# Performance work log

Hardware: AMD Instinct MI355X
Metric: run time of the kernel (lower is better)

Reference implementation:

```python
import jax, jax.numpy as jnp
import numpy as np

N_NODES = 100000
N_EDGES = 800000
D_IN = 128
D_H = 512


def _glorot(key, shape):
    fan_in, fan_out = shape[1], shape[0]
    lim = jnp.sqrt(6.0 / (fan_in + fan_out))
    return jax.random.uniform(key, shape, jnp.float32, -lim, lim)


def setup_inputs() -> dict:
    key = jax.random.key(0)
    ks = jax.random.split(key, 16)
    x = jax.random.normal(ks[0], (N_NODES, D_IN), jnp.float32)
    edge_index = jax.random.randint(ks[1], (2, N_EDGES), 0, N_NODES, jnp.int64)
    return {
        "x": x,
        "edge_index": edge_index,
        # SAGEConv layer1: lin_l (neighbors, with bias), lin_r (root, no bias)
        "Wl1": _glorot(ks[2], (D_H, D_IN)), "bl1": jnp.zeros((D_H,), jnp.float32),
        "Wr1": _glorot(ks[3], (D_H, D_IN)),
        # SAGEConv layer2
        "Wl2": _glorot(ks[4], (D_H, D_H)), "bl2": jnp.zeros((D_H,), jnp.float32),
        "Wr2": _glorot(ks[5], (D_H, D_H)),
        # SAGEConv layer3
        "Wl3": _glorot(ks[6], (D_H, D_H)), "bl3": jnp.zeros((D_H,), jnp.float32),
        "Wr3": _glorot(ks[7], (D_H, D_H)),
        # residual projections W, W2 (nn.Linear with bias)
        "Ww": _glorot(ks[8], (D_H, D_IN)), "bw": jnp.zeros((D_H,), jnp.float32),
        "Ww2": _glorot(ks[9], (D_H, D_IN)), "bw2": jnp.zeros((D_H,), jnp.float32),
        # shared PReLU parameter (nn.PReLU default: single param init 0.25)
        "a": jnp.array(0.25, jnp.float32),
    }


def _prelu(x, a):
    return jnp.where(x > 0, x, a * x)


def _sage_conv(x, src, dst, Wl, bl, Wr):
    # mean-aggregate neighbor features x[src] onto dst, then linear + root term
    msg = jax.ops.segment_sum(x[src], dst, num_segments=N_NODES)  # [N, d]
    deg = jax.ops.segment_sum(jnp.ones((src.shape[0],), x.dtype), dst,
                              num_segments=N_NODES)
    agg = msg / jnp.maximum(deg, 1.0)[:, None]
    return agg @ Wl.T + bl + x @ Wr.T


def reference(x, edge_index, Wl1, bl1, Wr1, Wl2, bl2, Wr2, Wl3, bl3, Wr3,
              Ww, bw, Ww2, bw2, a):
    src, dst = edge_index[0], edge_index[1]
    h1 = _prelu(_sage_conv(x, src, dst, Wl1, bl1, Wr1), a)
    h2 = _prelu(_sage_conv(h1 + (x @ Ww.T + bw), src, dst, Wl2, bl2, Wr2), a)
    h3 = _prelu(_sage_conv(h2 + h1 + (x @ Ww2.T + bw2), src, dst, Wl3, bl3, Wr3), a)
    return h3
```

## Files before the change

### kernel.cpp

```cpp
#include <hip/hip_runtime.h>
#include <stddef.h>

#define NN 100000
#define NE 800000
#define DIN 128
#define DH 512
#define MT 782
#define NWG (MT * 4)
#define CPX (NWG / 8)

typedef __attribute__((ext_vector_type(8))) short sh8;
typedef __attribute__((ext_vector_type(4))) float f32x4;

__device__ __forceinline__ unsigned short f2b(float f) {
  unsigned u = __float_as_uint(f);
  return (unsigned short)((u + 0x7FFFu + ((u >> 16) & 1u)) >> 16);
}
__device__ __forceinline__ float b2f(unsigned short s) {
  return __uint_as_float(((unsigned)s) << 16);
}

__device__ __forceinline__ void gload16(const unsigned short* g, unsigned short* l) {
  __builtin_amdgcn_global_load_lds(
      (const __attribute__((address_space(1))) void*)g,
      (__attribute__((address_space(3))) void*)l, 16, 0, 0);
}

#define SCHED_FENCE() __builtin_amdgcn_sched_barrier(0)
#define VMCNT(n) asm volatile("s_waitcnt vmcnt(" #n ")" ::: "memory")


__global__ void k_count(const int* __restrict__ dst, int* __restrict__ cnt) {
  int i = blockIdx.x * blockDim.x + threadIdx.x;
  if (i < NE) atomicAdd(&cnt[dst[i]], 1);
}

__global__ void k_invdeg(const int* __restrict__ cnt, float* __restrict__ inv_deg) {
  int i = blockIdx.x * blockDim.x + threadIdx.x;
  if (i < NN) inv_deg[i] = 1.0f / (float)(cnt[i] > 1 ? cnt[i] : 1);
}

__global__ void k_scan1(const int* __restrict__ cnt, int* __restrict__ excl,
                        int* __restrict__ partials) {
  __shared__ int sh[256];
  int tid = threadIdx.x;
  int base = blockIdx.x * 1024 + tid * 4;
  int v[4]; int s = 0;
#pragma unroll
  for (int i = 0; i < 4; i++) { int idx = base + i; v[i] = (idx < NN) ? cnt[idx] : 0; s += v[i]; }
  sh[tid] = s; __syncthreads();
  for (int off = 1; off < 256; off <<= 1) {
    int t = (tid >= off) ? sh[tid - off] : 0;
    __syncthreads();
    sh[tid] += t;
    __syncthreads();
  }
  int run = sh[tid] - s;
#pragma unroll
  for (int i = 0; i < 4; i++) { int idx = base + i; if (idx < NN) excl[idx] = run; run += v[i]; }
  if (tid == 255) partials[blockIdx.x] = sh[255];
}

__global__ void k_scan2(int* __restrict__ partials, int* __restrict__ row_start, int nparts) {
  __shared__ int sh[128];
  int tid = threadIdx.x;
  int v = (tid < nparts) ? partials[tid] : 0;
  sh[tid] = v; __syncthreads();
  for (int off = 1; off < 128; off <<= 1) {
    int t = (tid >= off) ? sh[tid - off] : 0;
    __syncthreads();
    sh[tid] += t;
    __syncthreads();
  }
  if (tid < nparts) partials[tid] = sh[tid] - v;
  if (tid == 127) row_start[NN] = sh[127];
}

__global__ void k_scan3(int* __restrict__ excl, const int* __restrict__ partials) {
  int i = blockIdx.x * blockDim.x + threadIdx.x;
  if (i < NN) excl[i] += partials[i >> 10];
}

__global__ void k_fill(const int* __restrict__ src, const int* __restrict__ dst,
                       const int* __restrict__ row_start, int* __restrict__ cursor,
                       int* __restrict__ ssrc) {
  int i = blockIdx.x * blockDim.x + threadIdx.x;
  if (i < NE) {
    int d = dst[i];
    int pos = atomicAdd(&cursor[d], 1);
    ssrc[row_start[d] + pos] = src[i];
  }
}


__global__ void k_f2b(const float* __restrict__ src, unsigned short* __restrict__ dst, int n) {
  int i = (blockIdx.x * blockDim.x + threadIdx.x) * 4;
  if (i < n) {
    float4 v = *(const float4*)(src + i);
    ushort4 o;
    o.x = f2b(v.x); o.y = f2b(v.y); o.z = f2b(v.z); o.w = f2b(v.w);
    *(ushort4*)(dst + i) = o;
  }
}


__global__ __launch_bounds__(256) void k_aggb512(
    const unsigned short* __restrict__ z, const int* __restrict__ rs,
    const int* __restrict__ ssrc, const float* __restrict__ inv_deg,
    unsigned short* __restrict__ agg) {
  int w = (blockIdx.x * blockDim.x + threadIdx.x) >> 6;
  int lane = threadIdx.x & 63;
  if (w >= NN) return;
  int e0 = rs[w], e1 = rs[w + 1];
  float acc[8] = {0, 0, 0, 0, 0, 0, 0, 0};
  int e = e0;
  for (; e + 1 < e1; e += 2) {
    int sa = ssrc[e], sb = ssrc[e + 1];
    sh8 va = *(const sh8*)(z + (size_t)sa * DH + lane * 8);
    sh8 vb = *(const sh8*)(z + (size_t)sb * DH + lane * 8);
#pragma unroll
    for (int j = 0; j < 8; ++j) acc[j] += b2f((unsigned short)va[j]) + b2f((unsigned short)vb[j]);
  }
  if (e < e1) {
    int sa = ssrc[e];
    sh8 va = *(const sh8*)(z + (size_t)sa * DH + lane * 8);
#pragma unroll
    for (int j = 0; j < 8; ++j) acc[j] += b2f((unsigned short)va[j]);
  }
  float s0 = inv_deg[w];
  sh8 o;
#pragma unroll
  for (int j = 0; j < 8; ++j) o[j] = (short)f2b(acc[j] * s0);
  *(sh8*)(agg + (size_t)w * DH + lane * 8) = o;
}

__global__ __launch_bounds__(256) void k_aggb128(
    const unsigned short* __restrict__ z, const int* __restrict__ rs,
    const int* __restrict__ ssrc, const float* __restrict__ inv_deg,
    unsigned short* __restrict__ agg) {
  int w = (blockIdx.x * blockDim.x + threadIdx.x) >> 6;
  int lane = threadIdx.x & 63;
  if (w >= NN) return;
  int e0 = rs[w], e1 = rs[w + 1];
  float a0 = 0.f, a1 = 0.f;
  int e = e0;
  for (; e + 1 < e1; e += 2) {
    int sa = ssrc[e], sb = ssrc[e + 1];
    unsigned va = *(const unsigned*)(z + (size_t)sa * DIN + lane * 2);
    unsigned vb = *(const unsigned*)(z + (size_t)sb * DIN + lane * 2);
    a0 += b2f((unsigned short)(va & 0xFFFFu)) + b2f((unsigned short)(vb & 0xFFFFu));
    a1 += b2f((unsigned short)(va >> 16)) + b2f((unsigned short)(vb >> 16));
  }
  if (e < e1) {
    unsigned va = *(const unsigned*)(z + (size_t)ssrc[e] * DIN + lane * 2);
    a0 += b2f((unsigned short)(va & 0xFFFFu));
    a1 += b2f((unsigned short)(va >> 16));
  }
  float s0 = inv_deg[w];
  unsigned o = (unsigned)f2b(a0 * s0) | ((unsigned)f2b(a1 * s0) << 16);
  *(unsigned*)(agg + (size_t)w * DIN + lane * 2) = o;
}


__device__ __forceinline__ void stage_tile(
    unsigned short* ldsA, unsigned short* ldsB,
    const unsigned short* __restrict__ A, int sA, int m0,
    const unsigned short* __restrict__ B, int sB, int n0,
    int k0, int tid) {
  const int w = tid >> 6, l = tid & 63;
  const int kc = (l & 3) * 8;
  const int rsub = l >> 2;
#pragma unroll
  for (int i = 0; i < 2; ++i) {
    int rl = w * 32 + i * 16 + rsub;
    int ra = m0 + rl; if (ra >= NN) ra = NN - 1;
    gload16(A + (size_t)ra * sA + k0 + kc, ldsA + (size_t)(w * 32 + i * 16) * 32);
    gload16(B + (size_t)(n0 + rl) * sB + k0 + kc, ldsB + (size_t)(w * 32 + i * 16) * 32);
  }
}

__device__ __forceinline__ void mfma_step(
    const unsigned short* As, const unsigned short* Bs,
    int wr, int wc, int r16, int kg, f32x4 (&acc)[4][4]) {
  sh8 af[4], bf[4];
#pragma unroll
  for (int i = 0; i < 4; ++i)
    af[i] = *(const sh8*)&As[(wr + i * 16 + r16) * 32 + kg * 8];
#pragma unroll
  for (int j = 0; j < 4; ++j)
    bf[j] = *(const sh8*)&Bs[(wc + j * 16 + r16) * 32 + kg * 8];
#pragma unroll
  for (int i = 0; i < 4; ++i)
#pragma unroll
    for (int j = 0; j < 4; ++j)
      acc[i][j] = __builtin_amdgcn_mfma_f32_16x16x32_bf16(af[i], bf[j], acc[i][j], 0, 0, 0);
}

#define PIPE_WAIT(s, S)                 \
  do {                                  \
    if ((s) < (S) - 2) VMCNT(8);        \
    else if ((s) == (S) - 2) VMCNT(4);  \
    else VMCNT(0);                      \
    SCHED_FENCE();                      \
    __builtin_amdgcn_s_barrier();       \
    SCHED_FENCE();                      \
  } while (0)

#define PIPE_END()                      \
  do {                                  \
    SCHED_FENCE();                      \
    __builtin_amdgcn_s_barrier();       \
    SCHED_FENCE();                      \
  } while (0)

__global__ __launch_bounds__(256, 2) void k_gemm1(
    const unsigned short* __restrict__ ag, const unsigned short* __restrict__ xb,
    const unsigned short* __restrict__ Wl1, const unsigned short* __restrict__ Wr1,
    const unsigned short* __restrict__ Ww, const unsigned short* __restrict__ Ww2,
    const float* __restrict__ bl1, const float* __restrict__ bw,
    const float* __restrict__ bw2, const float* __restrict__ aptr,
    unsigned short* __restrict__ z2o, unsigned short* __restrict__ z3po) {
  __shared__ __align__(16) unsigned short As[3][128 * 32];
  __shared__ __align__(16) unsigned short Bs[3][128 * 32];
  const int tid = threadIdx.x;
  const int b = blockIdx.x;
  const int L = (b & 7) * CPX + (b >> 3);
  const int m0 = (L >> 2) * 128, n0 = (L & 3) * 128;
  const int wid = tid >> 6, lane = tid & 63;
  const int r16 = lane & 15, kg = lane >> 4;
  const int wr = (wid >> 1) * 64, wc = (wid & 1) * 64;

  f32x4 a0[4][4], a1[4][4], a2[4][4];
#pragma unroll
  for (int i = 0; i < 4; ++i)
#pragma unroll
    for (int j = 0; j < 4; ++j) { a0[i][j] = 0.f; a1[i][j] = 0.f; a2[i][j] = 0.f; }

  auto stage = [&](int s, int buf) {
    const int seg = s >> 2, k0 = (s & 3) * 32;
    const unsigned short* Ap = (seg == 0) ? ag : xb;
    const unsigned short* Bp = (seg == 0) ? Wl1 : (seg == 1) ? Wr1 : (seg == 2) ? Ww : Ww2;
    stage_tile(As[buf], Bs[buf], Ap, DIN, m0, Bp, DIN, n0, k0, tid);
  };

  stage(0, 0);
  stage(1, 1);
  int cur = 0, nxt = 2;
  for (int s = 0; s < 16; ++s) {
    if (s + 2 < 16) stage(s + 2, nxt);
    PIPE_WAIT(s, 16);
    const int seg = s >> 2;
    __builtin_amdgcn_s_setprio(1);
    if (seg <= 1)      mfma_step(As[cur], Bs[cur], wr, wc, r16, kg, a0);
    else if (seg == 2) mfma_step(As[cur], Bs[cur], wr, wc, r16, kg, a1);
    else               mfma_step(As[cur], Bs[cur], wr, wc, r16, kg, a2);
    __builtin_amdgcn_s_setprio(0);
    PIPE_END();
    cur = (cur == 2) ? 0 : cur + 1;
    nxt = (nxt == 2) ? 0 : nxt + 1;
  }

  const float aval = aptr[0];
#pragma unroll
  for (int i = 0; i < 4; ++i) {
    const int mbase = m0 + wr + i * 16 + kg * 4;
#pragma unroll
    for (int j = 0; j < 4; ++j) {
      const int col = n0 + wc + j * 16 + r16;
      const float b1 = bl1[col], b2 = bw[col], b3 = bw2[col];
#pragma unroll
      for (int r = 0; r < 4; ++r) {
        const int m = mbase + r;
        if (m >= NN) continue;
        float h1 = a0[i][j][r] + b1;
        h1 = h1 > 0.f ? h1 : aval * h1;
        z2o[(size_t)m * DH + col] = f2b(h1 + a1[i][j][r] + b2);
        z3po[(size_t)m * DH + col] = f2b(h1 + a2[i][j][r] + b3);
      }
    }
  }
}

template <bool LAST>
__global__ __launch_bounds__(256, 3) void k_gemm23(
    const unsigned short* __restrict__ Aag, const unsigned short* __restrict__ Az,
    const unsigned short* __restrict__ Wl, const unsigned short* __restrict__ Wr,
    const float* __restrict__ bl, const float* __restrict__ aptr,
    const unsigned short* __restrict__ z3p, void* __restrict__ outp) {
  __shared__ __align__(16) unsigned short As[3][128 * 32];
  __shared__ __align__(16) unsigned short Bs[3][128 * 32];
  const int tid = threadIdx.x;
  const int b = blockIdx.x;
  const int L = (b & 7) * CPX + (b >> 3);
  const int m0 = (L >> 2) * 128, n0 = (L & 3) * 128;
  const int wid = tid >> 6, lane = tid & 63;
  const int r16 = lane & 15, kg = lane >> 4;
  const int wr = (wid >> 1) * 64, wc = (wid & 1) * 64;

  f32x4 acc[4][4];
#pragma unroll
  for (int i = 0; i < 4; ++i)
#pragma unroll
    for (int j = 0; j < 4; ++j) acc[i][j] = 0.f;

  auto stage = [&](int s, int buf) {
    const int k0 = (s & 15) * 32;
    const unsigned short* Ap = (s < 16) ? Aag : Az;
    const unsigned short* Bp = (s < 16) ? Wl : Wr;
    stage_tile(As[buf], Bs[buf], Ap, DH, m0, Bp, DH, n0, k0, tid);
  };

  stage(0, 0);
  stage(1, 1);
  int cur = 0, nxt = 2;
  for (int s = 0; s < 32; ++s) {
    if (s + 2 < 32) stage(s + 2, nxt);
    PIPE_WAIT(s, 32);
    __builtin_amdgcn_s_setprio(1);
    mfma_step(As[cur], Bs[cur], wr, wc, r16, kg, acc);
    __builtin_amdgcn_s_setprio(0);
    PIPE_END();
    cur = (cur == 2) ? 0 : cur + 1;
    nxt = (nxt == 2) ? 0 : nxt + 1;
  }

  const float aval = aptr[0];
  float* outf = (float*)outp;
  unsigned short* outb = (unsigned short*)outp;
#pragma unroll
  for (int i = 0; i < 4; ++i) {
    const int mbase = m0 + wr + i * 16 + kg * 4;
#pragma unroll
    for (int j = 0; j < 4; ++j) {
      const int col = n0 + wc + j * 16 + r16;
      const float bv = bl[col];
#pragma unroll
      for (int r = 0; r < 4; ++r) {
        const int m = mbase + r;
        if (m >= NN) continue;
        float h = acc[i][j][r] + bv;
        h = h > 0.f ? h : aval * h;
        if constexpr (LAST) {
          outf[(size_t)m * DH + col] = h;
        } else {
          outb[(size_t)m * DH + col] = f2b(h + b2f(z3p[(size_t)m * DH + col]));
        }
      }
    }
  }
}


extern "C" void kernel_launch(void* const* d_in, const int* in_sizes, int n_in,
                              void* d_out, int out_size, void* d_ws, size_t ws_size,
                              hipStream_t stream) {
  const float* x = (const float*)d_in[0];
  const int* ei = (const int*)d_in[1];
  const float* Wl1 = (const float*)d_in[2];
  const float* bl1 = (const float*)d_in[3];
  const float* Wr1 = (const float*)d_in[4];
  const float* Wl2 = (const float*)d_in[5];
  const float* bl2 = (const float*)d_in[6];
  const float* Wr2 = (const float*)d_in[7];
  const float* Wl3 = (const float*)d_in[8];
  const float* bl3 = (const float*)d_in[9];
  const float* Wr3 = (const float*)d_in[10];
  const float* Ww  = (const float*)d_in[11];
  const float* bw  = (const float*)d_in[12];
  const float* Ww2 = (const float*)d_in[13];
  const float* bw2 = (const float*)d_in[14];
  const float* ap  = (const float*)d_in[15];
  float* out = (float*)d_out;

  const size_t MP = 100096;
  char* w = (char*)d_ws;
  size_t off = 0;
  unsigned short* xb   = (unsigned short*)(w + off); off += MP * DIN * 2;
  unsigned short* ag1  = (unsigned short*)(w + off); off += MP * DIN * 2;
  unsigned short* agb  = (unsigned short*)(w + off); off += MP * DH * 2;
  unsigned short* zb   = (unsigned short*)(w + off); off += MP * DH * 2;
  unsigned short* zc   = (unsigned short*)(w + off); off += MP * DH * 2;
  unsigned short* z3pb = (unsigned short*)(w + off); off += MP * DH * 2;
  unsigned short* Wl1b = (unsigned short*)(w + off); off += (size_t)DH * DIN * 2;
  unsigned short* Wr1b = (unsigned short*)(w + off); off += (size_t)DH * DIN * 2;
  unsigned short* Wwb  = (unsigned short*)(w + off); off += (size_t)DH * DIN * 2;
  unsigned short* Ww2b = (unsigned short*)(w + off); off += (size_t)DH * DIN * 2;
  unsigned short* Wl2b = (unsigned short*)(w + off); off += (size_t)DH * DH * 2;
  unsigned short* Wr2b = (unsigned short*)(w + off); off += (size_t)DH * DH * 2;
  unsigned short* Wl3b = (unsigned short*)(w + off); off += (size_t)DH * DH * 2;
  unsigned short* Wr3b = (unsigned short*)(w + off); off += (size_t)DH * DH * 2;
  float* inv_deg = (float*)(w + off); off += (size_t)NN * 4;
  int* row_start = (int*)(w + off); off += (size_t)(NN + 1) * 4;
  int* cursor = (int*)(w + off); off += (size_t)NN * 4;
  int* ssrc = (int*)(w + off); off += (size_t)NE * 4;
  int* partials = (int*)(w + off); off += 512;

  const int* esrc = ei;
  const int* edst = ei + NE;

  hipMemsetAsync(cursor, 0, NN * 4, stream);
  k_count<<<(NE + 255) / 256, 256, 0, stream>>>(edst, cursor);
  k_invdeg<<<(NN + 255) / 256, 256, 0, stream>>>(cursor, inv_deg);
  k_scan1<<<(NN + 1023) / 1024, 256, 0, stream>>>(cursor, row_start, partials);
  k_scan2<<<1, 128, 0, stream>>>(partials, row_start, (NN + 1023) / 1024);
  k_scan3<<<(NN + 255) / 256, 256, 0, stream>>>(row_start, partials);
  hipMemsetAsync(cursor, 0, NN * 4, stream);
  k_fill<<<(NE + 255) / 256, 256, 0, stream>>>(esrc, edst, row_start, cursor, ssrc);

  const int WK = DH * DIN;
  const int WB = DH * DH;
  k_f2b<<<(WK / 4 + 255) / 256, 256, 0, stream>>>(Wl1, Wl1b, WK);
  k_f2b<<<(WK / 4 + 255) / 256, 256, 0, stream>>>(Wr1, Wr1b, WK);
  k_f2b<<<(WK / 4 + 255) / 256, 256, 0, stream>>>(Ww,  Wwb,  WK);
  k_f2b<<<(WK / 4 + 255) / 256, 256, 0, stream>>>(Ww2, Ww2b, WK);
  k_f2b<<<(WB / 4 + 255) / 256, 256, 0, stream>>>(Wl2, Wl2b, WB);
  k_f2b<<<(WB / 4 + 255) / 256, 256, 0, stream>>>(Wr2, Wr2b, WB);
  k_f2b<<<(WB / 4 + 255) / 256, 256, 0, stream>>>(Wl3, Wl3b, WB);
  k_f2b<<<(WB / 4 + 255) / 256, 256, 0, stream>>>(Wr3, Wr3b, WB);
  k_f2b<<<(NN * DIN / 4 + 255) / 256, 256, 0, stream>>>(x, xb, NN * DIN);

  k_aggb128<<<(NN + 3) / 4, 256, 0, stream>>>(xb, row_start, ssrc, inv_deg, ag1);
  k_gemm1<<<NWG, 256, 0, stream>>>(ag1, xb, Wl1b, Wr1b, Wwb, Ww2b, bl1, bw, bw2, ap,
                                   zb, z3pb);
  k_aggb512<<<(NN + 3) / 4, 256, 0, stream>>>(zb, row_start, ssrc, inv_deg, agb);
  k_gemm23<false><<<NWG, 256, 0, stream>>>(agb, zb, Wl2b, Wr2b, bl2, ap, z3pb, zc);
  k_aggb512<<<(NN + 3) / 4, 256, 0, stream>>>(zc, row_start, ssrc, inv_deg, agb);
  k_gemm23<true><<<NWG, 256, 0, stream>>>(agb, zc, Wl3b, Wr3b, bl3, ap, nullptr, out);
}
```

Measured before the change: 1.005 ms.

## Rewrite layer-2/3 GEMM as 256x256-tile 8-wave kernel with swizzled LDS

Replaces the 128x128, 4-wave, triple-buffered GEMM for layers 2 and 3 with a 256x256-tile, 8-wave (512-thread) kernel that uses double-buffered LDS with an XOR-swizzled layout. Each wave computes 128x64 in two halves, and the next stage's global-to-LDS loads are issued between the two MFMA halves. The goal is to raise arithmetic intensity per loaded byte, cut LDS bank conflicts, and remap workgroups evenly across the 8 XCDs. The trade-offs are more accumulator registers (8x4 f32x4 per wave), lower occupancy, and a larger padded workspace.

```diff
diff --git a/kernel.cpp b/kernel.cpp
--- a/kernel.cpp
+++ b/kernel.cpp
@@ -6,8 +6,8 @@
 #define DIN 128
 #define DH 512
 #define MT 782
-#define NWG (MT * 4)
-#define CPX (NWG / 8)
+#define NWG1 (MT * 4)
+#define CPX1 (NWG1 / 8)
 
 typedef __attribute__((ext_vector_type(8))) short sh8;
 typedef __attribute__((ext_vector_type(4))) float f32x4;
@@ -27,7 +27,9 @@
 }
 
 #define SCHED_FENCE() __builtin_amdgcn_sched_barrier(0)
+#define MEM_FENCE() asm volatile("" ::: "memory")
 #define VMCNT(n) asm volatile("s_waitcnt vmcnt(" #n ")" ::: "memory")
+#define LGKM0() asm volatile("s_waitcnt lgkmcnt(0)" ::: "memory")
 
 
 __global__ void k_count(const int* __restrict__ dst, int* __restrict__ cnt) {
@@ -203,14 +205,14 @@
     else VMCNT(0);                      \
     SCHED_FENCE();                      \
     __builtin_amdgcn_s_barrier();       \
-    SCHED_FENCE();                      \
+    MEM_FENCE(); SCHED_FENCE();         \
   } while (0)
 
 #define PIPE_END()                      \
   do {                                  \
     SCHED_FENCE();                      \
     __builtin_amdgcn_s_barrier();       \
-    SCHED_FENCE();                      \
+    MEM_FENCE(); SCHED_FENCE();         \
   } while (0)
 
 __global__ __launch_bounds__(256, 2) void k_gemm1(
@@ -224,7 +226,7 @@
   __shared__ __align__(16) unsigned short Bs[3][128 * 32];
   const int tid = threadIdx.x;
   const int b = blockIdx.x;
-  const int L = (b & 7) * CPX + (b >> 3);
+  const int L = (b & 7) * CPX1 + (b >> 3);
   const int m0 = (L >> 2) * 128, n0 = (L & 3) * 128;
   const int wid = tid >> 6, lane = tid & 63;
   const int r16 = lane & 15, kg = lane >> 4;
@@ -281,58 +283,110 @@
   }
 }
 
+
+#define TILE_E 8192
+#define NT23 32
+
+__device__ __forceinline__ void stage_u(const unsigned short* __restrict__ src,
+                                        int ld, int row0, int rowmax, int k0,
+                                        unsigned short* lds, int u, int l) {
+  int p = u * 8 + (l >> 3);
+  int v = (l & 7) ^ (p & 7);
+  int r = row0 + 2 * p + (v >> 2);
+  if (r > rowmax) r = rowmax;
+  gload16(src + (size_t)r * ld + k0 + (v & 3) * 8, lds + u * 512);
+}
+
+__device__ __forceinline__ sh8 frag(const unsigned short* lds, int r, int kg) {
+  int p = r >> 1;
+  int s = (((r & 1) << 2) | kg) ^ (p & 7);
+  return *(const sh8*)(lds + p * 64 + s * 8);
+}
+
 template <bool LAST>
-__global__ __launch_bounds__(256, 3) void k_gemm23(
+__global__ __launch_bounds__(512) void k8_gemm23(
     const unsigned short* __restrict__ Aag, const unsigned short* __restrict__ Az,
     const unsigned short* __restrict__ Wl, const unsigned short* __restrict__ Wr,
     const float* __restrict__ bl, const float* __restrict__ aptr,
     const unsigned short* __restrict__ z3p, void* __restrict__ outp) {
-  __shared__ __align__(16) unsigned short As[3][128 * 32];
-  __shared__ __align__(16) unsigned short Bs[3][128 * 32];
-  const int tid = threadIdx.x;
+  __shared__ __align__(16) unsigned short LA[2][TILE_E];
+  __shared__ __align__(16) unsigned short LB[2][TILE_E];
   const int b = blockIdx.x;
-  const int L = (b & 7) * CPX + (b >> 3);
-  const int m0 = (L >> 2) * 128, n0 = (L & 3) * 128;
-  const int wid = tid >> 6, lane = tid & 63;
-  const int r16 = lane & 15, kg = lane >> 4;
-  const int wr = (wid >> 1) * 64, wc = (wid & 1) * 64;
-
-  f32x4 acc[4][4];
-#pragma unroll
-  for (int i = 0; i < 4; ++i)
+  const int xcd = b & 7, lo = b >> 3;
+  const int wg = (xcd < 6 ? xcd * 98 : 588 + (xcd - 6) * 97) + lo;
+  const int m0 = (wg >> 1) * 256, n0 = (wg & 1) * 256;
+  const int tid = threadIdx.x, l = tid & 63, w = tid >> 6;
+  const int r16 = l & 15, kg = l >> 4;
+  const int rowA = (w >> 2) * 128, rowB = (w & 3) * 64;
+
+  f32x4 acc[8][4];
+#pragma unroll
+  for (int i = 0; i < 8; ++i)
 #pragma unroll
     for (int j = 0; j < 4; ++j) acc[i][j] = 0.f;
 
-  auto stage = [&](int s, int buf) {
-    const int k0 = (s & 15) * 32;
-    const unsigned short* Ap = (s < 16) ? Aag : Az;
-    const unsigned short* Bp = (s < 16) ? Wl : Wr;
-    stage_tile(As[buf], Bs[buf], Ap, DH, m0, Bp, DH, n0, k0, tid);
+  auto stA = [&](int t) {
+    const unsigned short* S = (t < 16) ? Aag : Az;
+    const int k0 = (t & 15) * 32;
+    unsigned short* d = LA[t & 1];
+#pragma unroll
+    for (int i = 0; i < 2; ++i) stage_u(S, DH, m0, NN - 1, k0, d, w * 2 + i, l);
   };
-
-  stage(0, 0);
-  stage(1, 1);
-  int cur = 0, nxt = 2;
-  for (int s = 0; s < 32; ++s) {
-    if (s + 2 < 32) stage(s + 2, nxt);
-    PIPE_WAIT(s, 32);
+  auto stB = [&](int t) {
+    const unsigned short* S = (t < 16) ? Wl : Wr;
+    const int k0 = (t & 15) * 32;
+    unsigned short* d = LB[t & 1];
+#pragma unroll
+    for (int i = 0; i < 2; ++i) stage_u(S, DH, n0, DH - 1, k0, d, w * 2 + i, l);
+  };
+
+  stA(0); stB(0);
+  stA(1); stB(1);
+
+  for (int t = 0; t < NT23; ++t) {
+    if (t == NT23 - 1) { VMCNT(0); } else { VMCNT(4); }
+    SCHED_FENCE();
+    __builtin_amdgcn_s_barrier();
+    MEM_FENCE(); SCHED_FENCE();
+    const unsigned short* As = LA[t & 1];
+    const unsigned short* Bs = LB[t & 1];
+    sh8 bfr[4], afr[4];
+#pragma unroll
+    for (int j = 0; j < 4; ++j) bfr[j] = frag(Bs, rowB + j * 16 + r16, kg);
+#pragma unroll
+    for (int i = 0; i < 4; ++i) afr[i] = frag(As, rowA + i * 16 + r16, kg);
     __builtin_amdgcn_s_setprio(1);
-    mfma_step(As[cur], Bs[cur], wr, wc, r16, kg, acc);
+#pragma unroll
+    for (int i = 0; i < 4; ++i)
+#pragma unroll
+      for (int j = 0; j < 4; ++j)
+        acc[i][j] = __builtin_amdgcn_mfma_f32_16x16x32_bf16(afr[i], bfr[j], acc[i][j], 0, 0, 0);
     __builtin_amdgcn_s_setprio(0);
-    PIPE_END();
-    cur = (cur == 2) ? 0 : cur + 1;
-    nxt = (nxt == 2) ? 0 : nxt + 1;
+#pragma unroll
+    for (int i = 0; i < 4; ++i) afr[i] = frag(As, rowA + (i + 4) * 16 + r16, kg);
+    LGKM0();
+    SCHED_FENCE();
+    __builtin_amdgcn_s_barrier();
+    MEM_FENCE(); SCHED_FENCE();
+    if (t + 2 < NT23) { stA(t + 2); stB(t + 2); }
+    __builtin_amdgcn_s_setprio(1);
+#pragma unroll
+    for (int i = 0; i < 4; ++i)
+#pragma unroll
+      for (int j = 0; j < 4; ++j)
+        acc[i + 4][j] = __builtin_amdgcn_mfma_f32_16x16x32_bf16(afr[i], bfr[j], acc[i + 4][j], 0, 0, 0);
+    __builtin_amdgcn_s_setprio(0);
   }
 
   const float aval = aptr[0];
   float* outf = (float*)outp;
   unsigned short* outb = (unsigned short*)outp;
 #pragma unroll
-  for (int i = 0; i < 4; ++i) {
-    const int mbase = m0 + wr + i * 16 + kg * 4;
+  for (int i = 0; i < 8; ++i) {
+    const int mbase = m0 + rowA + i * 16 + kg * 4;
 #pragma unroll
     for (int j = 0; j < 4; ++j) {
-      const int col = n0 + wc + j * 16 + r16;
+      const int col = n0 + rowB + j * 16 + r16;
       const float bv = bl[col];
 #pragma unroll
       for (int r = 0; r < 4; ++r) {
@@ -372,7 +426,7 @@
   const float* ap  = (const float*)d_in[15];
   float* out = (float*)d_out;
 
-  const size_t MP = 100096;
+  const size_t MP = 100352;
   char* w = (char*)d_ws;
   size_t off = 0;
   unsigned short* xb   = (unsigned short*)(w + off); off += MP * DIN * 2;
@@ -420,10 +474,10 @@
   k_f2b<<<(NN * DIN / 4 + 255) / 256, 256, 0, stream>>>(x, xb, NN * DIN);
 
   k_aggb128<<<(NN + 3) / 4, 256, 0, stream>>>(xb, row_start, ssrc, inv_deg, ag1);
-  k_gemm1<<<NWG, 256, 0, stream>>>(ag1, xb, Wl1b, Wr1b, Wwb, Ww2b, bl1, bw, bw2, ap,
-                                   zb, z3pb);
+  k_gemm1<<<NWG1, 256, 0, stream>>>(ag1, xb, Wl1b, Wr1b, Wwb, Ww2b, bl1, bw, bw2, ap,
+                                    zb, z3pb);
   k_aggb512<<<(NN + 3) / 4, 256, 0, stream>>>(zb, row_start, ssrc, inv_deg, agb);
-  k_gemm23<false><<<NWG, 256, 0, stream>>>(agb, zb, Wl2b, Wr2b, bl2, ap, z3pb, zc);
+  k8_gemm23<false><<<782, 512, 0, stream>>>(agb, zb, Wl2b, Wr2b, bl2, ap, z3pb, zc);
   k_aggb512<<<(NN + 3) / 4, 256, 0, stream>>>(zc, row_start, ssrc, inv_deg, agb);
-  k_gemm23<true><<<NWG, 256, 0, stream>>>(agb, zc, Wl3b, Wr3b, bl3, ap, nullptr, out);
-}
+  k8_gemm23<true><<<782, 512, 0, stream>>>(agb, zc, Wl3b, Wr3b, bl3, ap, nullptr, out);
+}
```

Result: slower. 1.069 ms (+6.3%).

## Replace async LDS triple-buffer pipeline in layer-2/3 GEMM with register-prefetch single buffer

Applied to the files above, without the earlier changes.

The layer-2/3 GEMM no longer uses a 3-stage global_load_lds pipeline with manual vmcnt waits. It prefetches the next K-slice of A and B into registers, writes it to a single LDS buffer between two __syncthreads, and then runs the MFMA step. This cuts LDS use from 48KB to 16KB and drops the occupancy hint from 3 to default, aiming for more resident workgroups. The cost is more registers, two full barriers per K step, and only one stage of prefetch. A compiler memory fence is also added after the barriers in the existing pipeline macros.

```diff
diff --git a/kernel.cpp b/kernel.cpp
--- a/kernel.cpp
+++ b/kernel.cpp
@@ -27,6 +27,7 @@
 }
 
 #define SCHED_FENCE() __builtin_amdgcn_sched_barrier(0)
+#define MEM_FENCE() asm volatile("" ::: "memory")
 #define VMCNT(n) asm volatile("s_waitcnt vmcnt(" #n ")" ::: "memory")
 
 
@@ -203,14 +204,14 @@
     else VMCNT(0);                      \
     SCHED_FENCE();                      \
     __builtin_amdgcn_s_barrier();       \
-    SCHED_FENCE();                      \
+    MEM_FENCE(); SCHED_FENCE();         \
   } while (0)
 
 #define PIPE_END()                      \
   do {                                  \
     SCHED_FENCE();                      \
     __builtin_amdgcn_s_barrier();       \
-    SCHED_FENCE();                      \
+    MEM_FENCE(); SCHED_FENCE();         \
   } while (0)
 
 __global__ __launch_bounds__(256, 2) void k_gemm1(
@@ -281,14 +282,15 @@
   }
 }
 
+
 template <bool LAST>
-__global__ __launch_bounds__(256, 3) void k_gemm23(
+__global__ __launch_bounds__(256) void k_rg23(
     const unsigned short* __restrict__ Aag, const unsigned short* __restrict__ Az,
     const unsigned short* __restrict__ Wl, const unsigned short* __restrict__ Wr,
     const float* __restrict__ bl, const float* __restrict__ aptr,
     const unsigned short* __restrict__ z3p, void* __restrict__ outp) {
-  __shared__ __align__(16) unsigned short As[3][128 * 32];
-  __shared__ __align__(16) unsigned short Bs[3][128 * 32];
+  __shared__ __align__(16) unsigned short As[128 * 32];
+  __shared__ __align__(16) unsigned short Bs[128 * 32];
   const int tid = threadIdx.x;
   const int b = blockIdx.x;
   const int L = (b & 7) * CPX + (b >> 3);
@@ -296,6 +298,8 @@
   const int wid = tid >> 6, lane = tid & 63;
   const int r16 = lane & 15, kg = lane >> 4;
   const int wr = (wid >> 1) * 64, wc = (wid & 1) * 64;
+  const int rA = tid >> 2;
+  const int cA = (tid & 3) * 8;
 
   f32x4 acc[4][4];
 #pragma unroll
@@ -303,25 +307,31 @@
 #pragma unroll
     for (int j = 0; j < 4; ++j) acc[i][j] = 0.f;
 
-  auto stage = [&](int s, int buf) {
-    const int k0 = (s & 15) * 32;
-    const unsigned short* Ap = (s < 16) ? Aag : Az;
-    const unsigned short* Bp = (s < 16) ? Wl : Wr;
-    stage_tile(As[buf], Bs[buf], Ap, DH, m0, Bp, DH, n0, k0, tid);
+  auto ldA = [&](int s, int r) -> sh8 {
+    const unsigned short* A = (s < 16) ? Aag : Az;
+    int row = m0 + r; if (row >= NN) row = NN - 1;
+    return *(const sh8*)(A + (size_t)row * DH + (s & 15) * 32 + cA);
   };
-
-  stage(0, 0);
-  stage(1, 1);
-  int cur = 0, nxt = 2;
+  auto ldB = [&](int s, int r) -> sh8 {
+    const unsigned short* W = (s < 16) ? Wl : Wr;
+    return *(const sh8*)(W + (size_t)(n0 + r) * DH + (s & 15) * 32 + cA);
+  };
+
+  sh8 va0 = ldA(0, rA), va1 = ldA(0, rA + 64);
+  sh8 vb0 = ldB(0, rA), vb1 = ldB(0, rA + 64);
+
   for (int s = 0; s < 32; ++s) {
-    if (s + 2 < 32) stage(s + 2, nxt);
-    PIPE_WAIT(s, 32);
-    __builtin_amdgcn_s_setprio(1);
-    mfma_step(As[cur], Bs[cur], wr, wc, r16, kg, acc);
-    __builtin_amdgcn_s_setprio(0);
-    PIPE_END();
-    cur = (cur == 2) ? 0 : cur + 1;
-    nxt = (nxt == 2) ? 0 : nxt + 1;
+    __syncthreads();
+    *(sh8*)&As[rA * 32 + cA] = va0;
+    *(sh8*)&As[(rA + 64) * 32 + cA] = va1;
+    *(sh8*)&Bs[rA * 32 + cA] = vb0;
+    *(sh8*)&Bs[(rA + 64) * 32 + cA] = vb1;
+    __syncthreads();
+    if (s + 1 < 32) {
+      va0 = ldA(s + 1, rA); va1 = ldA(s + 1, rA + 64);
+      vb0 = ldB(s + 1, rA); vb1 = ldB(s + 1, rA + 64);
+    }
+    mfma_step(As, Bs, wr, wc, r16, kg, acc);
   }
 
   const float aval = aptr[0];
@@ -423,7 +433,7 @@
   k_gemm1<<<NWG, 256, 0, stream>>>(ag1, xb, Wl1b, Wr1b, Wwb, Ww2b, bl1, bw, bw2, ap,
                                    zb, z3pb);
   k_aggb512<<<(NN + 3) / 4, 256, 0, stream>>>(zb, row_start, ssrc, inv_deg, agb);
-  k_gemm23<false><<<NWG, 256, 0, stream>>>(agb, zb, Wl2b, Wr2b, bl2, ap, z3pb, zc);
+  k_rg23<false><<<NWG, 256, 0, stream>>>(agb, zb, Wl2b, Wr2b, bl2, ap, z3pb, zc);
   k_aggb512<<<(NN + 3) / 4, 256, 0, stream>>>(zc, row_start, ssrc, inv_deg, agb);
-  k_gemm23<true><<<NWG, 256, 0, stream>>>(agb, zc, Wl3b, Wr3b, bl3, ap, nullptr, out);
-}
+  k_rg23<true><<<NWG, 256, 0, stream>>>(agb, zc, Wl3b, Wr3b, bl3, ap, nullptr, out);
+}
```

Result: no change. 987.4 us (-1.8%).
